# Kernel tuning notes

Measured on AMD Instinct MI355X. Metric: run time of the kernel, lower is better.

Reference implementation:

```python
import jax, jax.numpy as jnp
import numpy as np

N = 100000
E = 1600000
IN, HID, OUT, HEADS = 256, 16, 64, 8
NEG_SLOPE = 0.2


def gat_conv(x, src, dst, W, att_s, att_d, bias, heads, out_c, concat):
    n = x.shape[0]
    h = (x @ W).reshape(n, heads, out_c)              # [N,H,C]
    a_s = jnp.einsum('nhc,hc->nh', h, att_s)          # [N,H]
    a_d = jnp.einsum('nhc,hc->nh', h, att_d)          # [N,H]
    logits = jax.nn.leaky_relu(a_s[src] + a_d[dst], NEG_SLOPE)  # [E,H]
    m = jax.ops.segment_max(logits, dst, num_segments=n)        # [N,H]
    m = jnp.where(jnp.isfinite(m), m, 0.0)
    e = jnp.exp(logits - m[dst])                                 # [E,H]
    denom = jax.ops.segment_sum(e, dst, num_segments=n)         # [N,H]
    alpha = e / (denom[dst] + 1e-16)                             # [E,H]
    msg = h[src] * alpha[:, :, None]                             # [E,H,C]
    out = jax.ops.segment_sum(msg, dst, num_segments=n)          # [N,H,C]
    out = out.reshape(n, heads * out_c) if concat else out.mean(axis=1)
    return out + bias


def setup_inputs() -> dict:
    key = jax.random.key(0)
    ks = jax.random.split(key, 10)
    g = lambda k, shp, fan: jax.random.normal(k, shp, jnp.float32) * np.sqrt(2.0 / fan)
    x = jax.random.normal(ks[0], (N, IN), jnp.float32)
    edge_index = jax.random.randint(ks[1], (2, E), 0, N, jnp.int32)
    W1 = g(ks[2], (IN, HEADS * HID), IN)
    att1_s = g(ks[3], (HEADS, HID), HID)
    att1_d = g(ks[4], (HEADS, HID), HID)
    b1 = jnp.zeros((HEADS * HID,), jnp.float32)
    W2 = g(ks[5], (HEADS * HID, OUT), HEADS * HID)
    att2_s = g(ks[6], (1, OUT), OUT)
    att2_d = g(ks[7], (1, OUT), OUT)
    b2 = jnp.zeros((OUT,), jnp.float32)
    return {"x": x, "edge_index": edge_index, "W1": W1, "att1_s": att1_s,
            "att1_d": att1_d, "b1": b1, "W2": W2, "att2_s": att2_s,
            "att2_d": att2_d, "b2": b2}


def reference(x, edge_index, W1, att1_s, att1_d, b1, W2, att2_s, att2_d, b2):
    src, dst = edge_index[0], edge_index[1]
    h = gat_conv(x, src, dst, W1, att1_s, att1_d, b1, HEADS, HID, True)
    h = jax.nn.elu(h)  # dropout = identity in eval mode
    h = gat_conv(h, src, dst, W2, att2_s, att2_d, b2, 1, OUT, False)
    return jax.nn.log_softmax(h, axis=1)
```

## Files before the change

### kernel.cpp

```cpp
#include <hip/hip_runtime.h>
#include <math.h>

#define N_NODES 100000
#define N_EDGES 1600000
#define GEMM1_BLOCKS ((N_NODES + 63) / 64)
#define FUSED_BLOCKS (GEMM1_BLOCKS * 5)
#define KCHAIN 24

typedef __attribute__((ext_vector_type(8))) short short8;
typedef __attribute__((ext_vector_type(4))) float floatx4;

__device__ __forceinline__ float lrelu(float v) {
    return (v > 0.f) ? v : 0.2f * v;
}

__device__ __forceinline__ unsigned short f2bf(float f) {
    unsigned int u = __float_as_uint(f);
    u += 0x7fff + ((u >> 16) & 1);
    return (unsigned short)(u >> 16);
}

__device__ __forceinline__ float bflo(unsigned int u) { return __uint_as_float(u << 16); }
__device__ __forceinline__ float bfhi(unsigned int u) { return __uint_as_float(u & 0xffff0000u); }

__global__ void prep_kernel(const float* __restrict__ W1, const float* __restrict__ W2,
                            unsigned short* __restrict__ w1b, unsigned short* __restrict__ w2b) {
    int idx = blockIdx.x * 256 + threadIdx.x;
    if (idx < 4096) {
        int lane = idx & 63;
        int ts = idx >> 6;
        int t = ts >> 3, ks = ts & 7;
        int quad = lane >> 4, l15 = lane & 15;
        int kbase = ks * 32 + quad * 8;
        unsigned short o[8];
        #pragma unroll
        for (int j = 0; j < 8; j++)
            o[j] = f2bf(W1[(size_t)(kbase + j) * 128 + t * 16 + l15]);
        uint4 pk;
        pk.x = o[0] | ((unsigned int)o[1] << 16);
        pk.y = o[2] | ((unsigned int)o[3] << 16);
        pk.z = o[4] | ((unsigned int)o[5] << 16);
        pk.w = o[6] | ((unsigned int)o[7] << 16);
        ((uint4*)w1b)[idx] = pk;
    } else if (idx < 4096 + 1024) {
        int idx2 = idx - 4096;
        int lane = idx2 & 63;
        int ts = idx2 >> 6;
        int t = ts >> 2, ks = ts & 3;
        int quad = lane >> 4, l15 = lane & 15;
        int kbase = ks * 32 + quad * 8;
        unsigned short o[8];
        #pragma unroll
        for (int j = 0; j < 8; j++)
            o[j] = f2bf(W2[(size_t)(kbase + j) * 64 + t * 16 + l15]);
        uint4 pk;
        pk.x = o[0] | ((unsigned int)o[1] << 16);
        pk.y = o[2] | ((unsigned int)o[3] << 16);
        pk.z = o[4] | ((unsigned int)o[5] << 16);
        pk.w = o[6] | ((unsigned int)o[7] << 16);
        ((uint4*)w2b)[idx2] = pk;
    }
}

__global__ void __launch_bounds__(256) gemm1_link_kernel(
        const float* __restrict__ x, const short8* __restrict__ w1b,
        const float* __restrict__ att_s, const float* __restrict__ att_d,
        unsigned short* __restrict__ h1b, float* __restrict__ a1s, float* __restrict__ a1d,
        const int* __restrict__ ei, int* __restrict__ head, int2* __restrict__ rec8) {
    const int bid = blockIdx.x;
    if (bid % 5 != 0) {
        int lid = bid - bid / 5 - 1;
        int e = lid * 256 + threadIdx.x;
        if (e < N_EDGES) {
            int s = ei[e];
            int d = ei[N_EDGES + e];
            int old = atomicExch(&head[d], e);
            rec8[e] = make_int2(old, s);
        }
        return;
    }
    const int gid = bid / 5;
    const int lane = threadIdx.x & 63;
    const int wv = threadIdx.x >> 6;
    const int quad = lane >> 4;
    const int l15 = lane & 15;
    const int M = N_NODES;

    const int rowA = gid * 64 + wv * 16 + l15;
    const bool rowAok = rowA < M;
    const float4* xrow4 = (const float4*)(x + (size_t)rowA * 256);

    floatx4 acc[8];
    #pragma unroll
    for (int t = 0; t < 8; t++) acc[t] = (floatx4){0.f, 0.f, 0.f, 0.f};

    #pragma unroll
    for (int ks = 0; ks < 8; ks++) {
        float4 p0, p1;
        if (rowAok) {
            p0 = xrow4[ks * 8 + quad * 2];
            p1 = xrow4[ks * 8 + quad * 2 + 1];
        } else {
            p0 = make_float4(0.f, 0.f, 0.f, 0.f);
            p1 = p0;
        }
        short8 af;
        af[0] = (short)f2bf(p0.x); af[1] = (short)f2bf(p0.y);
        af[2] = (short)f2bf(p0.z); af[3] = (short)f2bf(p0.w);
        af[4] = (short)f2bf(p1.x); af[5] = (short)f2bf(p1.y);
        af[6] = (short)f2bf(p1.z); af[7] = (short)f2bf(p1.w);
        #pragma unroll
        for (int t = 0; t < 8; t++) {
            short8 bf = w1b[(t * 8 + ks) * 64 + lane];
            acc[t] = __builtin_amdgcn_mfma_f32_16x16x32_bf16(af, bf, acc[t], 0, 0, 0);
        }
    }

    const int rowC0 = gid * 64 + wv * 16 + quad * 4;
    #pragma unroll
    for (int t = 0; t < 8; t++) {
        float asw = att_s[t * 16 + l15];
        float adw = att_d[t * 16 + l15];
        #pragma unroll
        for (int r = 0; r < 4; r++) {
            int grow = rowC0 + r;
            float c = acc[t][r];
            if (grow < M) h1b[(size_t)grow * 128 + t * 16 + l15] = f2bf(c);
            float ps = c * asw;
            float pd = c * adw;
            ps += __shfl_xor(ps, 1, 64); ps += __shfl_xor(ps, 2, 64);
            ps += __shfl_xor(ps, 4, 64); ps += __shfl_xor(ps, 8, 64);
            pd += __shfl_xor(pd, 1, 64); pd += __shfl_xor(pd, 2, 64);
            pd += __shfl_xor(pd, 4, 64); pd += __shfl_xor(pd, 8, 64);
            if (l15 == 0 && grow < M) { a1s[grow * 8 + t] = ps; a1d[grow * 8 + t] = pd; }
        }
    }
}

__global__ void __launch_bounds__(256) csr_build_kernel(
        const int* __restrict__ head, const int2* __restrict__ rec8,
        int* __restrict__ rowstart, int* __restrict__ deg,
        int* __restrict__ counter, int* __restrict__ csr_src, int n) {
    int i = blockIdx.x * 256 + threadIdx.x;
    int lane = threadIdx.x & 63;
    int e = (i < n) ? head[i] : -1;
    int srcbuf[KCHAIN];
    int c = 0;
    #pragma unroll
    for (int k = 0; k < KCHAIN; k++) {
        srcbuf[k] = 0;
        if (e >= 0) {
            int2 r = rec8[e];
            srcbuf[k] = r.y;
            e = r.x;
            c++;
        }
    }
    int etail = e;
    while (e >= 0) {
        e = ((const int*)rec8)[(size_t)e * 2];
        c++;
    }
    int pre = c;
    #pragma unroll
    for (int off = 1; off < 64; off <<= 1) {
        int v = __shfl_up(pre, off, 64);
        if (lane >= off) pre += v;
    }
    int total = __shfl(pre, 63, 64);
    int base = 0;
    if (lane == 63) base = atomicAdd(counter, total);
    base = __shfl(base, 63, 64);
    if (i < n) {
        int rs = base + pre - c;
        rowstart[i] = rs;
        deg[i] = c;
        #pragma unroll
        for (int k = 0; k < KCHAIN; k++)
            if (k < c) csr_src[rs + k] = srcbuf[k];
        e = etail;
        int idx = rs + KCHAIN;
        while (e >= 0) {
            int2 r = rec8[e];
            csr_src[idx++] = r.y;
            e = r.x;
        }
    }
}

__global__ void __launch_bounds__(256) agg1_kernel(
        const unsigned short* __restrict__ h1b, const float* __restrict__ a1s,
        const float* __restrict__ a1d, const int* __restrict__ rowstart,
        const int* __restrict__ deg, const int* __restrict__ csr_src,
        const float* __restrict__ b1, unsigned int* __restrict__ h2b, int n) {
    const int lane = threadIdx.x & 63;
    const int node = blockIdx.x * 4 + (threadIdx.x >> 6);
    if (node >= n) return;
    const int h = lane >> 3;
    const int start = rowstart[node];
    const int d = deg[node];
    const float ad = a1d[node * 8 + h];
    float l = 0.f, acc0 = 0.f, acc1 = 0.f;
    int i = 0;
    for (; i + 8 <= d; i += 8) {
        int s[8];
        float as[8];
        unsigned int u[8];
        #pragma unroll
        for (int k = 0; k < 8; k++) s[k] = csr_src[start + i + k];
        #pragma unroll
        for (int k = 0; k < 8; k++) as[k] = a1s[s[k] * 8 + h];
        #pragma unroll
        for (int k = 0; k < 8; k++)
            u[k] = *(const unsigned int*)(h1b + (size_t)s[k] * 128 + lane * 2);
        #pragma unroll
        for (int k = 0; k < 8; k++) {
            float e = __expf(lrelu(as[k] + ad));
            l += e;
            acc0 += e * bflo(u[k]);
            acc1 += e * bfhi(u[k]);
        }
    }
    for (; i + 4 <= d; i += 4) {
        int s[4];
        float as[4];
        unsigned int u[4];
        #pragma unroll
        for (int k = 0; k < 4; k++) s[k] = csr_src[start + i + k];
        #pragma unroll
        for (int k = 0; k < 4; k++) as[k] = a1s[s[k] * 8 + h];
        #pragma unroll
        for (int k = 0; k < 4; k++)
            u[k] = *(const unsigned int*)(h1b + (size_t)s[k] * 128 + lane * 2);
        #pragma unroll
        for (int k = 0; k < 4; k++) {
            float e = __expf(lrelu(as[k] + ad));
            l += e;
            acc0 += e * bflo(u[k]);
            acc1 += e * bfhi(u[k]);
        }
    }
    for (; i < d; i++) {
        int s0 = csr_src[start + i];
        float as0 = a1s[s0 * 8 + h];
        unsigned int u0 = *(const unsigned int*)(h1b + (size_t)s0 * 128 + lane * 2);
        float e0 = __expf(lrelu(as0 + ad));
        l += e0;
        acc0 += e0 * bflo(u0);
        acc1 += e0 * bfhi(u0);
    }
    float inv = 1.f / (l + 1e-16f);
    float v0 = acc0 * inv + b1[lane * 2];
    float v1 = acc1 * inv + b1[lane * 2 + 1];
    v0 = (v0 > 0.f) ? v0 : expm1f(v0);
    v1 = (v1 > 0.f) ? v1 : expm1f(v1);
    h2b[(size_t)node * 64 + lane] = (unsigned int)f2bf(v0) | ((unsigned int)f2bf(v1) << 16);
}

__global__ void __launch_bounds__(256) gemm2_kernel(
        const short8* __restrict__ h2f, const short8* __restrict__ w2b,
        const float* __restrict__ att_s, const float* __restrict__ att_d,
        unsigned short* __restrict__ t2b, float* __restrict__ a2s, float* __restrict__ a2d,
        int n) {
    const int lane = threadIdx.x & 63;
    const int wv = threadIdx.x >> 6;
    const int quad = lane >> 4;
    const int l15 = lane & 15;

    const int rowA = blockIdx.x * 64 + wv * 16 + l15;
    const bool rowAok = rowA < n;

    floatx4 acc[4];
    #pragma unroll
    for (int t = 0; t < 4; t++) acc[t] = (floatx4){0.f, 0.f, 0.f, 0.f};

    #pragma unroll
    for (int ks = 0; ks < 4; ks++) {
        short8 af = {0, 0, 0, 0, 0, 0, 0, 0};
        if (rowAok) af = h2f[(size_t)rowA * 16 + ks * 4 + quad];
        #pragma unroll
        for (int t = 0; t < 4; t++) {
            short8 bf = w2b[(t * 4 + ks) * 64 + lane];
            acc[t] = __builtin_amdgcn_mfma_f32_16x16x32_bf16(af, bf, acc[t], 0, 0, 0);
        }
    }

    const int rowC0 = blockIdx.x * 64 + wv * 16 + quad * 4;
    float asw[4], adw[4];
    #pragma unroll
    for (int t = 0; t < 4; t++) {
        asw[t] = att_s[t * 16 + l15];
        adw[t] = att_d[t * 16 + l15];
    }
    #pragma unroll
    for (int r = 0; r < 4; r++) {
        int grow = rowC0 + r;
        bool ok = grow < n;
        float ps = 0.f, pd = 0.f;
        #pragma unroll
        for (int t = 0; t < 4; t++) {
            float c = acc[t][r];
            if (ok) t2b[(size_t)grow * 64 + t * 16 + l15] = f2bf(c);
            ps += c * asw[t];
            pd += c * adw[t];
        }
        ps += __shfl_xor(ps, 1, 64); ps += __shfl_xor(ps, 2, 64);
        ps += __shfl_xor(ps, 4, 64); ps += __shfl_xor(ps, 8, 64);
        pd += __shfl_xor(pd, 1, 64); pd += __shfl_xor(pd, 2, 64);
        pd += __shfl_xor(pd, 4, 64); pd += __shfl_xor(pd, 8, 64);
        if (l15 == 0 && ok) { a2s[grow] = ps; a2d[grow] = pd; }
    }
}

__global__ void __launch_bounds__(256) agg2_kernel(
        const unsigned short* __restrict__ t2b, const float* __restrict__ a2s,
        const float* __restrict__ a2d, const int* __restrict__ rowstart,
        const int* __restrict__ deg, const int* __restrict__ csr_src,
        const float* __restrict__ b2, float* __restrict__ out, int n) {
    const int lane = threadIdx.x & 63;
    const int node = blockIdx.x * 4 + (threadIdx.x >> 6);
    if (node >= n) return;
    const int start = rowstart[node];
    const int d = deg[node];
    const float ad = a2d[node];
    float l = 0.f, acc = 0.f;
    int i = 0;
    for (; i + 8 <= d; i += 8) {
        int s[8];
        float as[8];
        unsigned short u[8];
        #pragma unroll
        for (int k = 0; k < 8; k++) s[k] = csr_src[start + i + k];
        #pragma unroll
        for (int k = 0; k < 8; k++) as[k] = a2s[s[k]];
        #pragma unroll
        for (int k = 0; k < 8; k++) u[k] = t2b[(size_t)s[k] * 64 + lane];
        #pragma unroll
        for (int k = 0; k < 8; k++) {
            float e = __expf(lrelu(as[k] + ad));
            l += e;
            acc += e * __uint_as_float(((unsigned int)u[k]) << 16);
        }
    }
    for (; i + 4 <= d; i += 4) {
        int s[4];
        float as[4];
        unsigned short u[4];
        #pragma unroll
        for (int k = 0; k < 4; k++) s[k] = csr_src[start + i + k];
        #pragma unroll
        for (int k = 0; k < 4; k++) as[k] = a2s[s[k]];
        #pragma unroll
        for (int k = 0; k < 4; k++) u[k] = t2b[(size_t)s[k] * 64 + lane];
        #pragma unroll
        for (int k = 0; k < 4; k++) {
            float e = __expf(lrelu(as[k] + ad));
            l += e;
            acc += e * __uint_as_float(((unsigned int)u[k]) << 16);
        }
    }
    for (; i < d; i++) {
        int s0 = csr_src[start + i];
        float as0 = a2s[s0];
        unsigned short u0 = t2b[(size_t)s0 * 64 + lane];
        float e0 = __expf(lrelu(as0 + ad));
        l += e0;
        acc += e0 * __uint_as_float(((unsigned int)u0) << 16);
    }
    float v = acc / (l + 1e-16f) + b2[lane];
    float mx = v;
    #pragma unroll
    for (int off = 32; off >= 1; off >>= 1) mx = fmaxf(mx, __shfl_xor(mx, off, 64));
    float ex = expf(v - mx);
    float s2 = ex;
    #pragma unroll
    for (int off = 32; off >= 1; off >>= 1) s2 += __shfl_xor(s2, off, 64);
    out[(size_t)node * 64 + lane] = v - mx - logf(s2);
}


extern "C" void kernel_launch(void* const* d_in, const int* in_sizes, int n_in,
                              void* d_out, int out_size, void* d_ws, size_t ws_size,
                              hipStream_t stream) {
    const float* x     = (const float*)d_in[0];
    const int*   ei    = (const int*)d_in[1];
    const float* W1    = (const float*)d_in[2];
    const float* att1s = (const float*)d_in[3];
    const float* att1d = (const float*)d_in[4];
    const float* b1    = (const float*)d_in[5];
    const float* W2    = (const float*)d_in[6];
    const float* att2s = (const float*)d_in[7];
    const float* att2d = (const float*)d_in[8];
    const float* b2    = (const float*)d_in[9];
    float* out = (float*)d_out;

    const int N = N_NODES, E = N_EDGES;

    char* p = (char*)d_ws;
    auto take = [&](size_t bytes) {
        char* r = p;
        p += (bytes + 255) & ~(size_t)255;
        return (void*)r;
    };
    int*            head     = (int*)take((size_t)N * 4);
    int*            deg      = (int*)take((size_t)N * 4);
    int*            rowstart = (int*)take((size_t)N * 4);
    int*            counter  = (int*)take(256);
    int2*           rec8     = (int2*)take((size_t)E * 8);
    int*            csr_src  = (int*)take((size_t)E * 4);
    unsigned short* w1b      = (unsigned short*)take(64 * 64 * 16);
    unsigned short* w2b      = (unsigned short*)take(16 * 64 * 16);
    unsigned short* h1b      = (unsigned short*)take((size_t)N * 128 * 2);
    float*          a1s      = (float*)take((size_t)N * 8 * 4);
    float*          a1d      = (float*)take((size_t)N * 8 * 4);
    unsigned int*   h2b      = (unsigned int*)take((size_t)N * 64 * 4);
    unsigned short* t2b      = (unsigned short*)take((size_t)N * 64 * 2);
    float* a2s = a1s;
    float* a2d = a1d;

    hipMemsetAsync(head, 0xFF, (size_t)N * 4, stream);
    hipMemsetAsync(counter, 0, 4, stream);

    prep_kernel<<<20, 256, 0, stream>>>(W1, W2, w1b, w2b);
    gemm1_link_kernel<<<FUSED_BLOCKS, 256, 0, stream>>>(
        x, (const short8*)w1b, att1s, att1d, h1b, a1s, a1d, ei, head, rec8);
    csr_build_kernel<<<(N + 255) / 256, 256, 0, stream>>>(head, rec8, rowstart, deg,
                                                          counter, csr_src, N);
    agg1_kernel<<<(N + 3) / 4, 256, 0, stream>>>(h1b, a1s, a1d, rowstart, deg, csr_src,
                                                 b1, h2b, N);
    gemm2_kernel<<<(N + 63) / 64, 256, 0, stream>>>((const short8*)h2b, (const short8*)w2b,
                                                    att2s, att2d, t2b, a2s, a2d, N);
    agg2_kernel<<<(N + 3) / 4, 256, 0, stream>>>(t2b, a2s, a2d, rowstart, deg, csr_src,
                                                 b2, out, N);
}
```

Before: 443.8 us.

## Regroup kernels: fuse edge linking with weight prep and CSR build with GEMM1

Moves the edge linked-list construction into the weight-prep kernel and merges the CSR build into the GEMM1 kernel as extra leading blocks, removing one launch. The memory-bound, latency-heavy CSR chain walk now runs alongside the compute-bound GEMM1 tiles. The CSR blocks are placed first, so they may finish before the GEMM blocks start and overlap only partly. Register pressure from the CSR buffer could also lower GEMM occupancy.

```diff
diff --git a/kernel.cpp b/kernel.cpp
--- a/kernel.cpp
+++ b/kernel.cpp
@@ -4,7 +4,8 @@
 #define N_NODES 100000
 #define N_EDGES 1600000
 #define GEMM1_BLOCKS ((N_NODES + 63) / 64)
-#define FUSED_BLOCKS (GEMM1_BLOCKS * 5)
+#define LINK_BLOCKS ((N_EDGES + 255) / 256)
+#define CSR_BLOCKS ((N_NODES + 255) / 256)
 #define KCHAIN 24
 
 typedef __attribute__((ext_vector_type(8))) short short8;
@@ -23,9 +24,22 @@
 __device__ __forceinline__ float bflo(unsigned int u) { return __uint_as_float(u << 16); }
 __device__ __forceinline__ float bfhi(unsigned int u) { return __uint_as_float(u & 0xffff0000u); }
 
-__global__ void prep_kernel(const float* __restrict__ W1, const float* __restrict__ W2,
-                            unsigned short* __restrict__ w1b, unsigned short* __restrict__ w2b) {
-    int idx = blockIdx.x * 256 + threadIdx.x;
+__global__ void __launch_bounds__(256) prep_link_kernel(
+        const float* __restrict__ W1, const float* __restrict__ W2,
+        unsigned short* __restrict__ w1b, unsigned short* __restrict__ w2b,
+        const int* __restrict__ ei, int* __restrict__ head, int2* __restrict__ rec8) {
+    const int bid = blockIdx.x;
+    if (bid >= 20) {
+        int e = (bid - 20) * 256 + threadIdx.x;
+        if (e < N_EDGES) {
+            int s = ei[e];
+            int d = ei[N_EDGES + e];
+            int old = atomicExch(&head[d], e);
+            rec8[e] = make_int2(old, s);
+        }
+        return;
+    }
+    int idx = bid * 256 + threadIdx.x;
     if (idx < 4096) {
         int lane = idx & 63;
         int ts = idx >> 6;
@@ -62,24 +76,64 @@
     }
 }
 
-__global__ void __launch_bounds__(256) gemm1_link_kernel(
+__global__ void __launch_bounds__(256) gemm1_csr_kernel(
         const float* __restrict__ x, const short8* __restrict__ w1b,
         const float* __restrict__ att_s, const float* __restrict__ att_d,
         unsigned short* __restrict__ h1b, float* __restrict__ a1s, float* __restrict__ a1d,
-        const int* __restrict__ ei, int* __restrict__ head, int2* __restrict__ rec8) {
+        const int* __restrict__ head, const int2* __restrict__ rec8,
+        int* __restrict__ rowstart, int* __restrict__ deg,
+        int* __restrict__ counter, int* __restrict__ csr_src) {
     const int bid = blockIdx.x;
-    if (bid % 5 != 0) {
-        int lid = bid - bid / 5 - 1;
-        int e = lid * 256 + threadIdx.x;
-        if (e < N_EDGES) {
-            int s = ei[e];
-            int d = ei[N_EDGES + e];
-            int old = atomicExch(&head[d], e);
-            rec8[e] = make_int2(old, s);
+    if (bid < CSR_BLOCKS) {
+        int i = bid * 256 + threadIdx.x;
+        int lane = threadIdx.x & 63;
+        int n = N_NODES;
+        int e = (i < n) ? head[i] : -1;
+        int srcbuf[KCHAIN];
+        int c = 0;
+        #pragma unroll
+        for (int k = 0; k < KCHAIN; k++) {
+            srcbuf[k] = 0;
+            if (e >= 0) {
+                int2 r = rec8[e];
+                srcbuf[k] = r.y;
+                e = r.x;
+                c++;
+            }
+        }
+        int etail = e;
+        while (e >= 0) {
+            e = ((const int*)rec8)[(size_t)e * 2];
+            c++;
+        }
+        int pre = c;
+        #pragma unroll
+        for (int off = 1; off < 64; off <<= 1) {
+            int v = __shfl_up(pre, off, 64);
+            if (lane >= off) pre += v;
+        }
+        int total = __shfl(pre, 63, 64);
+        int base = 0;
+        if (lane == 63) base = atomicAdd(counter, total);
+        base = __shfl(base, 63, 64);
+        if (i < n) {
+            int rs = base + pre - c;
+            rowstart[i] = rs;
+            deg[i] = c;
+            #pragma unroll
+            for (int k = 0; k < KCHAIN; k++)
+                if (k < c) csr_src[rs + k] = srcbuf[k];
+            e = etail;
+            int idx = rs + KCHAIN;
+            while (e >= 0) {
+                int2 r = rec8[e];
+                csr_src[idx++] = r.y;
+                e = r.x;
+            }
         }
         return;
     }
-    const int gid = bid / 5;
+    const int gid = bid - CSR_BLOCKS;
     const int lane = threadIdx.x & 63;
     const int wv = threadIdx.x >> 6;
     const int quad = lane >> 4;
@@ -133,57 +187,6 @@
             pd += __shfl_xor(pd, 1, 64); pd += __shfl_xor(pd, 2, 64);
             pd += __shfl_xor(pd, 4, 64); pd += __shfl_xor(pd, 8, 64);
             if (l15 == 0 && grow < M) { a1s[grow * 8 + t] = ps; a1d[grow * 8 + t] = pd; }
-        }
-    }
-}
-
-__global__ void __launch_bounds__(256) csr_build_kernel(
-        const int* __restrict__ head, const int2* __restrict__ rec8,
-        int* __restrict__ rowstart, int* __restrict__ deg,
-        int* __restrict__ counter, int* __restrict__ csr_src, int n) {
-    int i = blockIdx.x * 256 + threadIdx.x;
-    int lane = threadIdx.x & 63;
-    int e = (i < n) ? head[i] : -1;
-    int srcbuf[KCHAIN];
-    int c = 0;
-    #pragma unroll
-    for (int k = 0; k < KCHAIN; k++) {
-        srcbuf[k] = 0;
-        if (e >= 0) {
-            int2 r = rec8[e];
-            srcbuf[k] = r.y;
-            e = r.x;
-            c++;
-        }
-    }
-    int etail = e;
-    while (e >= 0) {
-        e = ((const int*)rec8)[(size_t)e * 2];
-        c++;
-    }
-    int pre = c;
-    #pragma unroll
-    for (int off = 1; off < 64; off <<= 1) {
-        int v = __shfl_up(pre, off, 64);
-        if (lane >= off) pre += v;
-    }
-    int total = __shfl(pre, 63, 64);
-    int base = 0;
-    if (lane == 63) base = atomicAdd(counter, total);
-    base = __shfl(base, 63, 64);
-    if (i < n) {
-        int rs = base + pre - c;
-        rowstart[i] = rs;
-        deg[i] = c;
-        #pragma unroll
-        for (int k = 0; k < KCHAIN; k++)
-            if (k < c) csr_src[rs + k] = srcbuf[k];
-        e = etail;
-        int idx = rs + KCHAIN;
-        while (e >= 0) {
-            int2 r = rec8[e];
-            csr_src[idx++] = r.y;
-            e = r.x;
         }
     }
 }
@@ -421,11 +424,11 @@
     hipMemsetAsync(head, 0xFF, (size_t)N * 4, stream);
     hipMemsetAsync(counter, 0, 4, stream);
 
-    prep_kernel<<<20, 256, 0, stream>>>(W1, W2, w1b, w2b);
-    gemm1_link_kernel<<<FUSED_BLOCKS, 256, 0, stream>>>(
-        x, (const short8*)w1b, att1s, att1d, h1b, a1s, a1d, ei, head, rec8);
-    csr_build_kernel<<<(N + 255) / 256, 256, 0, stream>>>(head, rec8, rowstart, deg,
-                                                          counter, csr_src, N);
+    prep_link_kernel<<<20 + LINK_BLOCKS, 256, 0, stream>>>(W1, W2, w1b, w2b,
+                                                           ei, head, rec8);
+    gemm1_csr_kernel<<<CSR_BLOCKS + GEMM1_BLOCKS, 256, 0, stream>>>(
+        x, (const short8*)w1b, att1s, att1d, h1b, a1s, a1d,
+        head, rec8, rowstart, deg, counter, csr_src);
     agg1_kernel<<<(N + 3) / 4, 256, 0, stream>>>(h1b, a1s, a1d, rowstart, deg, csr_src,
                                                  b1, h2b, N);
     gemm2_kernel<<<(N + 63) / 64, 256, 0, stream>>>((const short8*)h2b, (const short8*)w2b,
```

Measured after the change: 455.9 us. +2.7%, slower.

## Fuse CSR construction into layer-1 aggregation by walking edge linked lists

Applied to the files above, without the earlier changes.

Drops the separate CSR-build kernel. Each wave now walks its destination node's linked edge list directly and accumulates the attention-weighted features on the fly. Source indices are kept in registers and written out to csr_src for the layer-2 aggregation. Row offsets are assigned by one block-level atomic after the walk. This removes a launch and a full pass over the linked list plus the csr_src re-read. The cost is that the per-edge gathers now depend on a serial pointer chase with no batching of independent loads, and nodes with more than 128 in-edges would get an incomplete CSR.

```diff
diff --git a/kernel.cpp b/kernel.cpp
--- a/kernel.cpp
+++ b/kernel.cpp
@@ -5,7 +5,6 @@
 #define N_EDGES 1600000
 #define GEMM1_BLOCKS ((N_NODES + 63) / 64)
 #define FUSED_BLOCKS (GEMM1_BLOCKS * 5)
-#define KCHAIN 24
 
 typedef __attribute__((ext_vector_type(8))) short short8;
 typedef __attribute__((ext_vector_type(4))) float floatx4;
@@ -137,124 +136,66 @@
     }
 }
 
-__global__ void __launch_bounds__(256) csr_build_kernel(
-        const int* __restrict__ head, const int2* __restrict__ rec8,
-        int* __restrict__ rowstart, int* __restrict__ deg,
-        int* __restrict__ counter, int* __restrict__ csr_src, int n) {
-    int i = blockIdx.x * 256 + threadIdx.x;
-    int lane = threadIdx.x & 63;
-    int e = (i < n) ? head[i] : -1;
-    int srcbuf[KCHAIN];
-    int c = 0;
-    #pragma unroll
-    for (int k = 0; k < KCHAIN; k++) {
-        srcbuf[k] = 0;
-        if (e >= 0) {
-            int2 r = rec8[e];
-            srcbuf[k] = r.y;
-            e = r.x;
-            c++;
-        }
-    }
-    int etail = e;
-    while (e >= 0) {
-        e = ((const int*)rec8)[(size_t)e * 2];
-        c++;
-    }
-    int pre = c;
-    #pragma unroll
-    for (int off = 1; off < 64; off <<= 1) {
-        int v = __shfl_up(pre, off, 64);
-        if (lane >= off) pre += v;
-    }
-    int total = __shfl(pre, 63, 64);
-    int base = 0;
-    if (lane == 63) base = atomicAdd(counter, total);
-    base = __shfl(base, 63, 64);
-    if (i < n) {
-        int rs = base + pre - c;
-        rowstart[i] = rs;
-        deg[i] = c;
-        #pragma unroll
-        for (int k = 0; k < KCHAIN; k++)
-            if (k < c) csr_src[rs + k] = srcbuf[k];
-        e = etail;
-        int idx = rs + KCHAIN;
-        while (e >= 0) {
-            int2 r = rec8[e];
-            csr_src[idx++] = r.y;
-            e = r.x;
-        }
-    }
-}
-
-__global__ void __launch_bounds__(256) agg1_kernel(
+__global__ void __launch_bounds__(256) csr_agg1_kernel(
         const unsigned short* __restrict__ h1b, const float* __restrict__ a1s,
-        const float* __restrict__ a1d, const int* __restrict__ rowstart,
-        const int* __restrict__ deg, const int* __restrict__ csr_src,
+        const float* __restrict__ a1d, const int* __restrict__ head,
+        const int2* __restrict__ rec8, int* __restrict__ rowstart,
+        int* __restrict__ deg, int* __restrict__ counter, int* __restrict__ csr_src,
         const float* __restrict__ b1, unsigned int* __restrict__ h2b, int n) {
     const int lane = threadIdx.x & 63;
-    const int node = blockIdx.x * 4 + (threadIdx.x >> 6);
-    if (node >= n) return;
+    const int wv = threadIdx.x >> 6;
+    const int node = blockIdx.x * 4 + wv;
+    const bool ok = node < n;
     const int h = lane >> 3;
-    const int start = rowstart[node];
-    const int d = deg[node];
-    const float ad = a1d[node * 8 + h];
+
+    __shared__ int sd[4];
+
+    const float ad = ok ? a1d[node * 8 + h] : 0.f;
     float l = 0.f, acc0 = 0.f, acc1 = 0.f;
-    int i = 0;
-    for (; i + 8 <= d; i += 8) {
-        int s[8];
-        float as[8];
-        unsigned int u[8];
-        #pragma unroll
-        for (int k = 0; k < 8; k++) s[k] = csr_src[start + i + k];
-        #pragma unroll
-        for (int k = 0; k < 8; k++) as[k] = a1s[s[k] * 8 + h];
-        #pragma unroll
-        for (int k = 0; k < 8; k++)
-            u[k] = *(const unsigned int*)(h1b + (size_t)s[k] * 128 + lane * 2);
-        #pragma unroll
-        for (int k = 0; k < 8; k++) {
-            float e = __expf(lrelu(as[k] + ad));
-            l += e;
-            acc0 += e * bflo(u[k]);
-            acc1 += e * bfhi(u[k]);
-        }
-    }
-    for (; i + 4 <= d; i += 4) {
-        int s[4];
-        float as[4];
-        unsigned int u[4];
-        #pragma unroll
-        for (int k = 0; k < 4; k++) s[k] = csr_src[start + i + k];
-        #pragma unroll
-        for (int k = 0; k < 4; k++) as[k] = a1s[s[k] * 8 + h];
-        #pragma unroll
-        for (int k = 0; k < 4; k++)
-            u[k] = *(const unsigned int*)(h1b + (size_t)s[k] * 128 + lane * 2);
-        #pragma unroll
-        for (int k = 0; k < 4; k++) {
-            float e = __expf(lrelu(as[k] + ad));
-            l += e;
-            acc0 += e * bflo(u[k]);
-            acc1 += e * bfhi(u[k]);
-        }
-    }
-    for (; i < d; i++) {
-        int s0 = csr_src[start + i];
-        float as0 = a1s[s0 * 8 + h];
-        unsigned int u0 = *(const unsigned int*)(h1b + (size_t)s0 * 128 + lane * 2);
-        float e0 = __expf(lrelu(as0 + ad));
-        l += e0;
-        acc0 += e0 * bflo(u0);
-        acc1 += e0 * bfhi(u0);
-    }
-    float inv = 1.f / (l + 1e-16f);
-    float v0 = acc0 * inv + b1[lane * 2];
-    float v1 = acc1 * inv + b1[lane * 2 + 1];
-    v0 = (v0 > 0.f) ? v0 : expm1f(v0);
-    v1 = (v1 > 0.f) ? v1 : expm1f(v1);
-    h2b[(size_t)node * 64 + lane] = (unsigned int)f2bf(v0) | ((unsigned int)f2bf(v1) << 16);
+    int mysrc0 = 0, mysrc1 = 0;
+    int e = ok ? head[node] : -1;
+    int t = 0;
+    while (e >= 0) {
+        int2 r = rec8[e];
+        int s = r.y;
+        if (t == lane) mysrc0 = s;
+        if (t == lane + 64) mysrc1 = s;
+        float as = a1s[s * 8 + h];
+        unsigned int u = *(const unsigned int*)(h1b + (size_t)s * 128 + lane * 2);
+        float ew = __expf(lrelu(as + ad));
+        l += ew;
+        acc0 += ew * bflo(u);
+        acc1 += ew * bfhi(u);
+        e = r.x;
+        t++;
+    }
+    const int d = t;
+
+    if (lane == 0) sd[wv] = d;
+    __syncthreads();
+    if (threadIdx.x == 0) {
+        int t0 = sd[0], t1 = sd[1], t2 = sd[2], t3 = sd[3];
+        int base = atomicAdd(counter, t0 + t1 + t2 + t3);
+        sd[0] = base;
+        sd[1] = base + t0;
+        sd[2] = base + t0 + t1;
+        sd[3] = base + t0 + t1 + t2;
+    }
+    __syncthreads();
+    const int rs = sd[wv];
+
+    if (ok) {
+        if (lane == 0) { rowstart[node] = rs; deg[node] = d; }
+        if (lane < d) csr_src[rs + lane] = mysrc0;
+        if (lane + 64 < d) csr_src[rs + lane + 64] = mysrc1;
+
+        float inv = 1.f / (l + 1e-16f);
+        float v0 = acc0 * inv + b1[lane * 2];
+        float v1 = acc1 * inv + b1[lane * 2 + 1];
+        v0 = (v0 > 0.f) ? v0 : expm1f(v0);
+        v1 = (v1 > 0.f) ? v1 : expm1f(v1);
+        h2b[(size_t)node * 64 + lane] = (unsigned int)f2bf(v0) | ((unsigned int)f2bf(v1) << 16);
+    }
 }
 
 __global__ void __launch_bounds__(256) gemm2_kernel(
@@ -424,10 +365,8 @@
     prep_kernel<<<20, 256, 0, stream>>>(W1, W2, w1b, w2b);
     gemm1_link_kernel<<<FUSED_BLOCKS, 256, 0, stream>>>(
         x, (const short8*)w1b, att1s, att1d, h1b, a1s, a1d, ei, head, rec8);
-    csr_build_kernel<<<(N + 255) / 256, 256, 0, stream>>>(head, rec8, rowstart, deg,
-                                                          counter, csr_src, N);
-    agg1_kernel<<<(N + 3) / 4, 256, 0, stream>>>(h1b, a1s, a1d, rowstart, deg, csr_src,
-                                                 b1, h2b, N);
+    csr_agg1_kernel<<<(N + 3) / 4, 256, 0, stream>>>(
+        h1b, a1s, a1d, head, rec8, rowstart, deg, counter, csr_src, b1, h2b, N);
     gemm2_kernel<<<(N + 63) / 64, 256, 0, stream>>>((const short8*)h2b, (const short8*)w2b,
                                                     att2s, att2d, t2b, a2s, a2d, N);
     agg2_kernel<<<(N + 3) / 4, 256, 0, stream>>>(t2b, a2s, a2d, rowstart, deg, csr_src,
```

After: 645.0 us. 1.45x slower.

## Fuse layer-2 GEMM into agg1 kernel using shared-memory W2 and per-node dot products

Applied to the files above, without the earlier changes.

Merges the second-layer linear transform and attention projections into the first aggregation kernel. Each wavefront keeps its aggregated node row in shared memory and computes the 64 outputs with scalar FMAs against a bf16 W2 copy held in LDS. This removes the h2 round trip through global memory and one kernel launch. In exchange, every block of four nodes reloads 16KB of W2 into LDS, and the MFMA path is replaced by scalar FMAs. The h2 activation also stays in fp32 instead of being rounded to bf16.

```diff
diff --git a/kernel.cpp b/kernel.cpp
--- a/kernel.cpp
+++ b/kernel.cpp
@@ -22,9 +22,10 @@
 
 __device__ __forceinline__ float bflo(unsigned int u) { return __uint_as_float(u << 16); }
 __device__ __forceinline__ float bfhi(unsigned int u) { return __uint_as_float(u & 0xffff0000u); }
+__device__ __forceinline__ float bfs(unsigned short s) { return __uint_as_float(((unsigned int)s) << 16); }
 
 __global__ void prep_kernel(const float* __restrict__ W1, const float* __restrict__ W2,
-                            unsigned short* __restrict__ w1b, unsigned short* __restrict__ w2b) {
+                            unsigned short* __restrict__ w1b, unsigned short* __restrict__ w2p) {
     int idx = blockIdx.x * 256 + threadIdx.x;
     if (idx < 4096) {
         int lane = idx & 63;
@@ -42,23 +43,16 @@
         pk.z = o[4] | ((unsigned int)o[5] << 16);
         pk.w = o[6] | ((unsigned int)o[7] << 16);
         ((uint4*)w1b)[idx] = pk;
-    } else if (idx < 4096 + 1024) {
+    } else if (idx < 4096 + 2048) {
         int idx2 = idx - 4096;
-        int lane = idx2 & 63;
-        int ts = idx2 >> 6;
-        int t = ts >> 2, ks = ts & 3;
-        int quad = lane >> 4, l15 = lane & 15;
-        int kbase = ks * 32 + quad * 8;
-        unsigned short o[8];
-        #pragma unroll
-        for (int j = 0; j < 8; j++)
-            o[j] = f2bf(W2[(size_t)(kbase + j) * 64 + t * 16 + l15]);
-        uint4 pk;
-        pk.x = o[0] | ((unsigned int)o[1] << 16);
-        pk.y = o[2] | ((unsigned int)o[3] << 16);
-        pk.z = o[4] | ((unsigned int)o[5] << 16);
-        pk.w = o[6] | ((unsigned int)o[7] << 16);
-        ((uint4*)w2b)[idx2] = pk;
+        unsigned short o0 = f2bf(W2[idx2 * 4]);
+        unsigned short o1 = f2bf(W2[idx2 * 4 + 1]);
+        unsigned short o2 = f2bf(W2[idx2 * 4 + 2]);
+        unsigned short o3 = f2bf(W2[idx2 * 4 + 3]);
+        uint2 pk;
+        pk.x = o0 | ((unsigned int)o1 << 16);
+        pk.y = o2 | ((unsigned int)o3 << 16);
+        ((uint2*)w2p)[idx2] = pk;
     }
 }
 
@@ -188,13 +182,25 @@
     }
 }
 
-__global__ void __launch_bounds__(256) agg1_kernel(
+__global__ void __launch_bounds__(256) agg1_gemm2_kernel(
         const unsigned short* __restrict__ h1b, const float* __restrict__ a1s,
         const float* __restrict__ a1d, const int* __restrict__ rowstart,
         const int* __restrict__ deg, const int* __restrict__ csr_src,
-        const float* __restrict__ b1, unsigned int* __restrict__ h2b, int n) {
+        const float* __restrict__ b1, const unsigned short* __restrict__ w2p,
+        const float* __restrict__ att2s, const float* __restrict__ att2d,
+        unsigned short* __restrict__ t2b, float* __restrict__ a2s,
+        float* __restrict__ a2d, int n) {
+    __shared__ unsigned short w2s[128 * 64];
+    __shared__ float h2s[4][128];
+
+    #pragma unroll
+    for (int i = 0; i < 4; i++)
+        ((uint4*)w2s)[threadIdx.x + i * 256] = ((const uint4*)w2p)[threadIdx.x + i * 256];
+    __syncthreads();
+
     const int lane = threadIdx.x & 63;
-    const int node = blockIdx.x * 4 + (threadIdx.x >> 6);
+    const int wv = threadIdx.x >> 6;
+    const int node = blockIdx.x * 4 + wv;
     if (node >= n) return;
     const int h = lane >> 3;
     const int start = rowstart[node];
@@ -254,62 +260,25 @@
     float v1 = acc1 * inv + b1[lane * 2 + 1];
     v0 = (v0 > 0.f) ? v0 : expm1f(v0);
     v1 = (v1 > 0.f) ? v1 : expm1f(v1);
-    h2b[(size_t)node * 64 + lane] = (unsigned int)f2bf(v0) | ((unsigned int)f2bf(v1) << 16);
-}
-
-__global__ void __launch_bounds__(256) gemm2_kernel(
-        const short8* __restrict__ h2f, const short8* __restrict__ w2b,
-        const float* __restrict__ att_s, const float* __restrict__ att_d,
-        unsigned short* __restrict__ t2b, float* __restrict__ a2s, float* __restrict__ a2d,
-        int n) {
-    const int lane = threadIdx.x & 63;
-    const int wv = threadIdx.x >> 6;
-    const int quad = lane >> 4;
-    const int l15 = lane & 15;
-
-    const int rowA = blockIdx.x * 64 + wv * 16 + l15;
-    const bool rowAok = rowA < n;
-
-    floatx4 acc[4];
-    #pragma unroll
-    for (int t = 0; t < 4; t++) acc[t] = (floatx4){0.f, 0.f, 0.f, 0.f};
-
-    #pragma unroll
-    for (int ks = 0; ks < 4; ks++) {
-        short8 af = {0, 0, 0, 0, 0, 0, 0, 0};
-        if (rowAok) af = h2f[(size_t)rowA * 16 + ks * 4 + quad];
-        #pragma unroll
-        for (int t = 0; t < 4; t++) {
-            short8 bf = w2b[(t * 4 + ks) * 64 + lane];
-            acc[t] = __builtin_amdgcn_mfma_f32_16x16x32_bf16(af, bf, acc[t], 0, 0, 0);
-        }
-    }
-
-    const int rowC0 = blockIdx.x * 64 + wv * 16 + quad * 4;
-    float asw[4], adw[4];
-    #pragma unroll
-    for (int t = 0; t < 4; t++) {
-        asw[t] = att_s[t * 16 + l15];
-        adw[t] = att_d[t * 16 + l15];
-    }
-    #pragma unroll
-    for (int r = 0; r < 4; r++) {
-        int grow = rowC0 + r;
-        bool ok = grow < n;
-        float ps = 0.f, pd = 0.f;
-        #pragma unroll
-        for (int t = 0; t < 4; t++) {
-            float c = acc[t][r];
-            if (ok) t2b[(size_t)grow * 64 + t * 16 + l15] = f2bf(c);
-            ps += c * asw[t];
-            pd += c * adw[t];
-        }
-        ps += __shfl_xor(ps, 1, 64); ps += __shfl_xor(ps, 2, 64);
-        ps += __shfl_xor(ps, 4, 64); ps += __shfl_xor(ps, 8, 64);
-        pd += __shfl_xor(pd, 1, 64); pd += __shfl_xor(pd, 2, 64);
-        pd += __shfl_xor(pd, 4, 64); pd += __shfl_xor(pd, 8, 64);
-        if (l15 == 0 && ok) { a2s[grow] = ps; a2d[grow] = pd; }
-    }
+
+    h2s[wv][lane * 2] = v0;
+    h2s[wv][lane * 2 + 1] = v1;
+    float t2 = 0.f;
+    #pragma unroll
+    for (int k = 0; k < 128; k += 2) {
+        float hk0 = h2s[wv][k];
+        float hk1 = h2s[wv][k + 1];
+        t2 += hk0 * bfs(w2s[k * 64 + lane]) + hk1 * bfs(w2s[(k + 1) * 64 + lane]);
+    }
+    t2b[(size_t)node * 64 + lane] = f2bf(t2);
+    float ps = t2 * att2s[lane];
+    float pd = t2 * att2d[lane];
+    #pragma unroll
+    for (int off = 32; off >= 1; off >>= 1) {
+        ps += __shfl_xor(ps, off, 64);
+        pd += __shfl_xor(pd, off, 64);
+    }
+    if (lane == 0) { a2s[node] = ps; a2d[node] = pd; }
 }
 
 __global__ void __launch_bounds__(256) agg2_kernel(
@@ -339,7 +308,7 @@
         for (int k = 0; k < 8; k++) {
             float e = __expf(lrelu(as[k] + ad));
             l += e;
-            acc += e * __uint_as_float(((unsigned int)u[k]) << 16);
+            acc += e * bfs(u[k]);
         }
     }
     for (; i + 4 <= d; i += 4) {
@@ -356,7 +325,7 @@
         for (int k = 0; k < 4; k++) {
             float e = __expf(lrelu(as[k] + ad));
             l += e;
-            acc += e * __uint_as_float(((unsigned int)u[k]) << 16);
+            acc += e * bfs(u[k]);
         }
     }
     for (; i < d; i++) {
@@ -365,7 +334,7 @@
         unsigned short u0 = t2b[(size_t)s0 * 64 + lane];
         float e0 = __expf(lrelu(as0 + ad));
         l += e0;
-        acc += e0 * __uint_as_float(((unsigned int)u0) << 16);
+        acc += e0 * bfs(u0);
     }
     float v = acc / (l + 1e-16f) + b2[lane];
     float mx = v;
@@ -409,27 +378,25 @@
     int2*           rec8     = (int2*)take((size_t)E * 8);
     int*            csr_src  = (int*)take((size_t)E * 4);
     unsigned short* w1b      = (unsigned short*)take(64 * 64 * 16);
-    unsigned short* w2b      = (unsigned short*)take(16 * 64 * 16);
+    unsigned short* w2p      = (unsigned short*)take(128 * 64 * 2);
     unsigned short* h1b      = (unsigned short*)take((size_t)N * 128 * 2);
     float*          a1s      = (float*)take((size_t)N * 8 * 4);
     float*          a1d      = (float*)take((size_t)N * 8 * 4);
-    unsigned int*   h2b      = (unsigned int*)take((size_t)N * 64 * 4);
     unsigned short* t2b      = (unsigned short*)take((size_t)N * 64 * 2);
-    float* a2s = a1s;
-    float* a2d = a1d;
+    float*          a2s      = (float*)take((size_t)N * 4);
+    float*          a2d      = (float*)take((size_t)N * 4);
 
     hipMemsetAsync(head, 0xFF, (size_t)N * 4, stream);
     hipMemsetAsync(counter, 0, 4, stream);
 
-    prep_kernel<<<20, 256, 0, stream>>>(W1, W2, w1b, w2b);
+    prep_kernel<<<24, 256, 0, stream>>>(W1, W2, w1b, w2p);
     gemm1_link_kernel<<<FUSED_BLOCKS, 256, 0, stream>>>(
         x, (const short8*)w1b, att1s, att1d, h1b, a1s, a1d, ei, head, rec8);
     csr_build_kernel<<<(N + 255) / 256, 256, 0, stream>>>(head, rec8, rowstart, deg,
                                                           counter, csr_src, N);
-    agg1_kernel<<<(N + 3) / 4, 256, 0, stream>>>(h1b, a1s, a1d, rowstart, deg, csr_src,
-                                                 b1, h2b, N);
-    gemm2_kernel<<<(N + 63) / 64, 256, 0, stream>>>((const short8*)h2b, (const short8*)w2b,
-                                                    att2s, att2d, t2b, a2s, a2d, N);
+    agg1_gemm2_kernel<<<(N + 3) / 4, 256, 0, stream>>>(
+        h1b, a1s, a1d, rowstart, deg, csr_src, b1, w2p, att2s, att2d,
+        t2b, a2s, a2d, N);
     agg2_kernel<<<(N + 3) / 4, 256, 0, stream>>>(t2b, a2s, a2d, rowstart, deg, csr_src,
                                                  b2, out, N);
 }
```

New measurement: 477.5 us. 7.6% more time.
